# Optimization experiments

Hardware: AMD Instinct MI355X
Metric: run time of the kernel (lower is better)

The kernel has to match this reference:

```python
import jax, jax.numpy as jnp
import numpy as np
import math

D_IN, D_OUT, Q, K = 256, 64, 128, 6
BATCH, S = 2, 1024

def setup_inputs() -> dict:
    key = jax.random.key(0)
    ks = jax.random.split(key, 7)
    X0 = jax.random.normal(ks[0], (BATCH, S, D_IN), dtype=jnp.float32)
    t = jax.random.uniform(ks[1], (BATCH, 1), dtype=jnp.float32)
    lim = 1.0 / math.sqrt(D_IN)
    Wc_w = jax.random.uniform(ks[2], (Q, D_IN), minval=-lim, maxval=lim, dtype=jnp.float32)
    Wc_b = jax.random.uniform(ks[3], (Q,), minval=-lim, maxval=lim, dtype=jnp.float32)
    w = jax.random.normal(ks[4], (Q,), dtype=jnp.float32)
    A = jax.random.normal(ks[5], (D_OUT, Q, K), dtype=jnp.float32) / math.sqrt(Q * K)
    Bp = jax.random.uniform(ks[6], (D_OUT, Q, K), dtype=jnp.float32) * (2.0 * math.pi)
    return {"X0": X0, "t": t, "Wc_w": Wc_w, "Wc_b": Wc_b, "w": w, "A": A, "Bp": Bp}

def reference(X0, t, Wc_w, Wc_b, w, A, Bp):
    # v(t) = sum_{q,k} A[d,q,k] * sin(k*(C_q(x) + w_q*t) + B[d,q,k])
    k_vec = jnp.arange(1, K + 1, dtype=X0.dtype)  # [K]
    C = jnp.einsum('bsi,qi->bsq', X0, Wc_w) + Wc_b          # [B,S,Q]
    angle = C + (w[None, :] * t)[:, None, :]                # [B,S,Q]
    angle_k = angle[..., None] * k_vec                      # [B,S,Q,K]
    # sin(angle_k + B) = sin(angle_k)*cos(B) + cos(angle_k)*sin(B)
    # avoids materializing the [B,S,D_out,Q,K] tensor of the naive form.
    V = (jnp.einsum('bsqk,dqk->bsd', jnp.sin(angle_k), A * jnp.cos(Bp))
         + jnp.einsum('bsqk,dqk->bsd', jnp.cos(angle_k), A * jnp.sin(Bp)))
    return V
```

## Files before the change

kernel.cpp:

```cpp
#include <hip/hip_runtime.h>
#include <hip/hip_bf16.h>
#include <string.h>


#define D_IN  256
#define D_OUT 64
#define NQ    128
#define NK    6
#define NB    2
#define NS    1024
#define NM    (NB*NS)
#define KJ    (NQ*NK*2)
#define GSTR  392

typedef __attribute__((ext_vector_type(8))) short short8;
typedef __attribute__((ext_vector_type(4))) float floatx4;

#define W2_OFF 0

__device__ inline unsigned short f2bf(float x) {
    __hip_bfloat16 h = __float2bfloat16(x);
    unsigned short u;
    memcpy(&u, &h, sizeof(u));
    return u;
}

__device__ inline unsigned int pack2bf(float lo, float hi) {
    return (unsigned int)f2bf(lo) | ((unsigned int)f2bf(hi) << 16);
}

__device__ inline short8 cvt8(float4 a, float4 b) {
    short8 r;
    r[0] = (short)f2bf(a.x); r[1] = (short)f2bf(a.y);
    r[2] = (short)f2bf(a.z); r[3] = (short)f2bf(a.w);
    r[4] = (short)f2bf(b.x); r[5] = (short)f2bf(b.y);
    r[6] = (short)f2bf(b.z); r[7] = (short)f2bf(b.w);
    return r;
}

__global__ __launch_bounds__(256) void prep_kernel(const float* __restrict__ A,
                                                   const float* __restrict__ Bp,
                                                   unsigned short* __restrict__ W2) {
    const int i = blockIdx.x * blockDim.x + threadIdx.x;
    if (i >= D_OUT * NQ * NK) return;
    const int d = i / (NQ * NK);
    const int r = i % (NQ * NK);
    const int q = r / NK;
    const int k = r % NK;
    float s, c;
    __sincosf(Bp[i], &s, &c);
    const float a = A[i];
    W2[(size_t)d * KJ + q * 12 + 2 * k]     = f2bf(a * c);
    W2[(size_t)d * KJ + q * 12 + 2 * k + 1] = f2bf(a * s);
}

__global__ __launch_bounds__(256) void fused_kernel(
        const float* __restrict__ X0, const float* __restrict__ Wc_w,
        const float* __restrict__ Wc_b, const float* __restrict__ wq,
        const float* __restrict__ t, const short* __restrict__ W2,
        float* __restrict__ out) {
    const int m0   = (blockIdx.x >> 1) * 16;
    const int d0   = (blockIdx.x & 1) * 32;
    const int wv   = threadIdx.x >> 6;
    const int lane = threadIdx.x & 63;
    const int lm   = lane & 15;
    const int quad = lane >> 4;

    __shared__ short Gl[4 * 16 * GSTR];
    __shared__ float red[4][64][9];

    floatx4 acc1[2] = {floatx4{0,0,0,0}, floatx4{0,0,0,0}};
    const int q0 = wv * 32;
    const float* xrow = X0 + (size_t)(m0 + lm) * D_IN + quad * 8;
#pragma unroll
    for (int k0 = 0; k0 < D_IN; k0 += 32) {
        const float4* xp = (const float4*)(xrow + k0);
        short8 a = cvt8(xp[0], xp[1]);
#pragma unroll
        for (int nt = 0; nt < 2; ++nt) {
            const float4* wp = (const float4*)(Wc_w + (size_t)(q0 + nt * 16 + lm) * D_IN
                                               + k0 + quad * 8);
            short8 b = cvt8(wp[0], wp[1]);
            acc1[nt] = __builtin_amdgcn_mfma_f32_16x16x32_bf16(a, b, acc1[nt], 0, 0, 0);
        }
    }

    const float tb = t[m0 / NS];
    short* gbase = Gl + wv * 16 * GSTR;
#pragma unroll
    for (int nt = 0; nt < 2; ++nt) {
        const int q = q0 + nt * 16 + lm;
        const float base = Wc_b[q] + wq[q] * tb;
#pragma unroll
        for (int r = 0; r < 4; ++r) {
            const int m = quad * 4 + r;
            const float ang = acc1[nt][r] + base;
            float s1, c1;
            __sincosf(ang, &s1, &c1);
            unsigned int p[6];
            p[0] = pack2bf(s1, c1);
            float sk = s1, ck = c1;
#pragma unroll
            for (int k = 1; k < NK; ++k) {
                const float sn = sk * c1 + ck * s1;
                const float cn = ck * c1 - sk * s1;
                p[k] = pack2bf(sn, cn);
                sk = sn; ck = cn;
            }
            uint2* dst = reinterpret_cast<uint2*>(gbase + m * GSTR + (nt * 16 + lm) * 12);
            dst[0] = make_uint2(p[0], p[1]);
            dst[1] = make_uint2(p[2], p[3]);
            dst[2] = make_uint2(p[4], p[5]);
        }
    }

    floatx4 acc2[2] = {floatx4{0,0,0,0}, floatx4{0,0,0,0}};
    const short* gw = gbase + lm * GSTR + quad * 8;
    const int j0 = wv * (KJ / 4);
#pragma unroll
    for (int it = 0; it < KJ / 4 / 32; ++it) {
        short8 a = *(const short8*)(gw + it * 32);
#pragma unroll
        for (int nt = 0; nt < 2; ++nt) {
            short8 b = *(const short8*)(W2 + (size_t)(d0 + nt * 16 + lm) * KJ
                                        + j0 + it * 32 + quad * 8);
            acc2[nt] = __builtin_amdgcn_mfma_f32_16x16x32_bf16(a, b, acc2[nt], 0, 0, 0);
        }
    }

#pragma unroll
    for (int nt = 0; nt < 2; ++nt)
#pragma unroll
        for (int r = 0; r < 4; ++r)
            red[wv][lane][nt * 4 + r] = acc2[nt][r];
    __syncthreads();

#pragma unroll
    for (int jj = 0; jj < 2; ++jj) {
        const int j  = wv * 2 + jj;
        const int nt = j >> 2;
        const int r  = j & 3;
        const float v = red[0][lane][j] + red[1][lane][j]
                      + red[2][lane][j] + red[3][lane][j];
        out[(size_t)(m0 + quad * 4 + r) * D_OUT + d0 + nt * 16 + lm] = v;
    }
}

extern "C" void kernel_launch(void* const* d_in, const int* in_sizes, int n_in,
                              void* d_out, int out_size, void* d_ws, size_t ws_size,
                              hipStream_t stream) {
    const float* X0   = (const float*)d_in[0];
    const float* t    = (const float*)d_in[1];
    const float* Wc_w = (const float*)d_in[2];
    const float* Wc_b = (const float*)d_in[3];
    const float* w    = (const float*)d_in[4];
    const float* A    = (const float*)d_in[5];
    const float* Bp   = (const float*)d_in[6];
    float* out = (float*)d_out;

    unsigned short* W2 = (unsigned short*)((char*)d_ws + W2_OFF);

    prep_kernel<<<(D_OUT * NQ * NK + 255) / 256, 256, 0, stream>>>(A, Bp, W2);
    fused_kernel<<<(NM / 16) * 2, 256, 0, stream>>>(X0, Wc_w, Wc_b, w, t,
                                                    (const short*)W2, out);
}
```

Before: 76.18 us.

## Pre-convert X0 and Wc_w to bf16 in prep kernel, split output across four blocks

The prep kernel now also converts X0 and Wc_w to bf16 in the workspace, so the fused kernel loads ready-made bf16 fragments instead of converting fp32 per block. The fused grid grows from 256 to 512 blocks, each handling 16 output columns instead of 32, which raises parallelism but makes every block recompute the first GEMM and the sin/cos expansion four times instead of twice. A barrier is added after the LDS writes. The extra conversion pass costs additional global traffic before the main kernel.

```diff
diff --git a/kernel.cpp b/kernel.cpp
--- a/kernel.cpp
+++ b/kernel.cpp
@@ -16,7 +16,9 @@
 typedef __attribute__((ext_vector_type(8))) short short8;
 typedef __attribute__((ext_vector_type(4))) float floatx4;
 
-#define W2_OFF 0
+#define W2_SOFF   0
+#define WCW_SOFF  (D_OUT * KJ)
+#define XBF_SOFF  (WCW_SOFF + NQ * D_IN)
 
 __device__ inline unsigned short f2bf(float x) {
     __hip_bfloat16 h = __float2bfloat16(x);
@@ -29,58 +31,68 @@
     return (unsigned int)f2bf(lo) | ((unsigned int)f2bf(hi) << 16);
 }
 
-__device__ inline short8 cvt8(float4 a, float4 b) {
-    short8 r;
-    r[0] = (short)f2bf(a.x); r[1] = (short)f2bf(a.y);
-    r[2] = (short)f2bf(a.z); r[3] = (short)f2bf(a.w);
-    r[4] = (short)f2bf(b.x); r[5] = (short)f2bf(b.y);
-    r[6] = (short)f2bf(b.z); r[7] = (short)f2bf(b.w);
-    return r;
-}
-
 __global__ __launch_bounds__(256) void prep_kernel(const float* __restrict__ A,
                                                    const float* __restrict__ Bp,
-                                                   unsigned short* __restrict__ W2) {
-    const int i = blockIdx.x * blockDim.x + threadIdx.x;
-    if (i >= D_OUT * NQ * NK) return;
-    const int d = i / (NQ * NK);
-    const int r = i % (NQ * NK);
-    const int q = r / NK;
-    const int k = r % NK;
-    float s, c;
-    __sincosf(Bp[i], &s, &c);
-    const float a = A[i];
-    W2[(size_t)d * KJ + q * 12 + 2 * k]     = f2bf(a * c);
-    W2[(size_t)d * KJ + q * 12 + 2 * k + 1] = f2bf(a * s);
+                                                   const float* __restrict__ Wc_w,
+                                                   const float* __restrict__ X0,
+                                                   unsigned short* __restrict__ ws) {
+    const int bid = blockIdx.x;
+    const int tid = threadIdx.x;
+    if (bid < 192) {
+        const int i = bid * 256 + tid;
+        const int d = i / (NQ * NK);
+        const int r = i % (NQ * NK);
+        const int q = r / NK;
+        const int k = r % NK;
+        float s, c;
+        __sincosf(Bp[i], &s, &c);
+        const float a = A[i];
+        unsigned short* W2 = ws + W2_SOFF;
+        W2[(size_t)d * KJ + q * 12 + 2 * k]     = f2bf(a * c);
+        W2[(size_t)d * KJ + q * 12 + 2 * k + 1] = f2bf(a * s);
+    } else if (bid < 224) {
+        const int i4 = (bid - 192) * 256 + tid;
+        const float4 v = ((const float4*)Wc_w)[i4];
+        ushort4 o;
+        o.x = f2bf(v.x); o.y = f2bf(v.y); o.z = f2bf(v.z); o.w = f2bf(v.w);
+        ((ushort4*)(ws + WCW_SOFF))[i4] = o;
+    } else {
+        const int i4 = (bid - 224) * 256 + tid;
+        const float4 v = ((const float4*)X0)[i4];
+        ushort4 o;
+        o.x = f2bf(v.x); o.y = f2bf(v.y); o.z = f2bf(v.z); o.w = f2bf(v.w);
+        ((ushort4*)(ws + XBF_SOFF))[i4] = o;
+    }
 }
 
 __global__ __launch_bounds__(256) void fused_kernel(
-        const float* __restrict__ X0, const float* __restrict__ Wc_w,
+        const unsigned short* __restrict__ ws,
         const float* __restrict__ Wc_b, const float* __restrict__ wq,
-        const float* __restrict__ t, const short* __restrict__ W2,
-        float* __restrict__ out) {
-    const int m0   = (blockIdx.x >> 1) * 16;
-    const int d0   = (blockIdx.x & 1) * 32;
+        const float* __restrict__ t, float* __restrict__ out) {
+    const int m0   = (blockIdx.x >> 2) * 16;
+    const int d0   = (blockIdx.x & 3) * 16;
     const int wv   = threadIdx.x >> 6;
     const int lane = threadIdx.x & 63;
     const int lm   = lane & 15;
     const int quad = lane >> 4;
 
     __shared__ short Gl[4 * 16 * GSTR];
-    __shared__ float red[4][64][9];
+    __shared__ float red[4][64][5];
+
+    const unsigned short* W2  = ws + W2_SOFF;
+    const unsigned short* Wcw = ws + WCW_SOFF;
+    const unsigned short* Xbf = ws + XBF_SOFF;
 
     floatx4 acc1[2] = {floatx4{0,0,0,0}, floatx4{0,0,0,0}};
     const int q0 = wv * 32;
-    const float* xrow = X0 + (size_t)(m0 + lm) * D_IN + quad * 8;
+    const unsigned short* xrow = Xbf + (size_t)(m0 + lm) * D_IN + quad * 8;
 #pragma unroll
     for (int k0 = 0; k0 < D_IN; k0 += 32) {
-        const float4* xp = (const float4*)(xrow + k0);
-        short8 a = cvt8(xp[0], xp[1]);
+        short8 a = *(const short8*)(xrow + k0);
 #pragma unroll
         for (int nt = 0; nt < 2; ++nt) {
-            const float4* wp = (const float4*)(Wc_w + (size_t)(q0 + nt * 16 + lm) * D_IN
-                                               + k0 + quad * 8);
-            short8 b = cvt8(wp[0], wp[1]);
+            short8 b = *(const short8*)(Wcw + (size_t)(q0 + nt * 16 + lm) * D_IN
+                                        + k0 + quad * 8);
             acc1[nt] = __builtin_amdgcn_mfma_f32_16x16x32_bf16(a, b, acc1[nt], 0, 0, 0);
         }
     }
@@ -113,36 +125,29 @@
             dst[2] = make_uint2(p[4], p[5]);
         }
     }
+    __syncthreads();
 
-    floatx4 acc2[2] = {floatx4{0,0,0,0}, floatx4{0,0,0,0}};
+    floatx4 acc2 = {0.f, 0.f, 0.f, 0.f};
     const short* gw = gbase + lm * GSTR + quad * 8;
     const int j0 = wv * (KJ / 4);
 #pragma unroll
     for (int it = 0; it < KJ / 4 / 32; ++it) {
         short8 a = *(const short8*)(gw + it * 32);
-#pragma unroll
-        for (int nt = 0; nt < 2; ++nt) {
-            short8 b = *(const short8*)(W2 + (size_t)(d0 + nt * 16 + lm) * KJ
-                                        + j0 + it * 32 + quad * 8);
-            acc2[nt] = __builtin_amdgcn_mfma_f32_16x16x32_bf16(a, b, acc2[nt], 0, 0, 0);
-        }
+        short8 b = *(const short8*)((const short*)W2 + (size_t)(d0 + lm) * KJ
+                                    + j0 + it * 32 + quad * 8);
+        acc2 = __builtin_amdgcn_mfma_f32_16x16x32_bf16(a, b, acc2, 0, 0, 0);
     }
 
 #pragma unroll
-    for (int nt = 0; nt < 2; ++nt)
-#pragma unroll
-        for (int r = 0; r < 4; ++r)
-            red[wv][lane][nt * 4 + r] = acc2[nt][r];
+    for (int r = 0; r < 4; ++r)
+        red[wv][lane][r] = acc2[r];
     __syncthreads();
 
-#pragma unroll
-    for (int jj = 0; jj < 2; ++jj) {
-        const int j  = wv * 2 + jj;
-        const int nt = j >> 2;
-        const int r  = j & 3;
-        const float v = red[0][lane][j] + red[1][lane][j]
-                      + red[2][lane][j] + red[3][lane][j];
-        out[(size_t)(m0 + quad * 4 + r) * D_OUT + d0 + nt * 16 + lm] = v;
+    {
+        const int r = wv;
+        const float v = red[0][lane][r] + red[1][lane][r]
+                      + red[2][lane][r] + red[3][lane][r];
+        out[(size_t)(m0 + quad * 4 + r) * D_OUT + d0 + lm] = v;
     }
 }
 
@@ -158,9 +163,8 @@
     const float* Bp   = (const float*)d_in[6];
     float* out = (float*)d_out;
 
-    unsigned short* W2 = (unsigned short*)((char*)d_ws + W2_OFF);
+    unsigned short* ws = (unsigned short*)d_ws;
 
-    prep_kernel<<<(D_OUT * NQ * NK + 255) / 256, 256, 0, stream>>>(A, Bp, W2);
-    fused_kernel<<<(NM / 16) * 2, 256, 0, stream>>>(X0, Wc_w, Wc_b, w, t,
-                                                    (const short*)W2, out);
+    prep_kernel<<<736, 256, 0, stream>>>(A, Bp, Wc_w, X0, ws);
+    fused_kernel<<<512, 256, 0, stream>>>(ws, Wc_b, w, t, out);
 }
```

After: 76.96 us. About the same (+1.0%).
